# Optimization experiments

Measured on AMD Instinct MI355X. Metric: run time of the kernel, lower is better.

The kernel has to match this reference:

```python
import jax, jax.numpy as jnp
import numpy as np

N_NODES = 50000
N_EDGES = 800000
IN_DIM = 128
HID = 128
NUM_CLASSES = 2


def setup_inputs() -> dict:
    key = jax.random.key(0)
    ks = jax.random.split(key, 16)
    inp = {
        "adj_row": jax.random.randint(ks[0], (N_EDGES,), 0, N_NODES),
        "adj_col": jax.random.randint(ks[1], (N_EDGES,), 0, N_NODES),
        "adj_vals": jax.random.uniform(ks[2], (N_EDGES,), dtype=jnp.float32),
        "input_feature": jax.random.normal(ks[3], (N_NODES, IN_DIM), dtype=jnp.float32),
        "graph_indicator": jax.random.randint(ks[4], (N_NODES,), 0, 64),
        # GCN layer params (kaiming-uniform-ish init; zeros bias like the torch module)
        "W1": jax.random.uniform(ks[5], (IN_DIM, HID), jnp.float32, -1, 1) * np.sqrt(6.0 / IN_DIM),
        "b1": jnp.zeros((HID,), jnp.float32),
        "W2": jax.random.uniform(ks[6], (HID, HID), jnp.float32, -1, 1) * np.sqrt(6.0 / HID),
        "b2": jnp.zeros((HID,), jnp.float32),
        "W3": jax.random.uniform(ks[7], (HID, HID), jnp.float32, -1, 1) * np.sqrt(6.0 / HID),
        "b3": jnp.zeros((HID,), jnp.float32),
        # fc params (torch.nn.Linear default init range)
        "fcW1": jax.random.uniform(ks[8], (3 * HID, HID), jnp.float32, -1, 1) / np.sqrt(3 * HID),
        "fcb1": jax.random.uniform(ks[9], (HID,), jnp.float32, -1, 1) / np.sqrt(3 * HID),
        "fcW2": jax.random.uniform(ks[10], (HID, HID // 2), jnp.float32, -1, 1) / np.sqrt(HID),
        "fcb2": jax.random.uniform(ks[11], (HID // 2,), jnp.float32, -1, 1) / np.sqrt(HID),
        "fcW3": jax.random.uniform(ks[12], (HID // 2, NUM_CLASSES), jnp.float32, -1, 1) / np.sqrt(HID // 2),
        "fcb3": jax.random.uniform(ks[13], (NUM_CLASSES,), jnp.float32, -1, 1) / np.sqrt(HID // 2),
    }
    return inp


def _gcn_layer(row, col, vals, x, W, b, n_nodes):
    # support = X @ W  -> dense GEMM
    support = x @ W
    # sparse.mm(A, support): out[i] = sum_{e: row[e]=i} vals[e] * support[col[e]]
    msgs = support[col] * vals[:, None]  # [E, D] gather + scale
    agg = jax.ops.segment_sum(msgs, row, num_segments=n_nodes)
    return agg + b


def reference(adj_row, adj_col, adj_vals, input_feature, graph_indicator,
              W1, b1, W2, b2, W3, b3, fcW1, fcb1, fcW2, fcb2, fcW3, fcb3):
    n = input_feature.shape[0]
    g1 = jax.nn.relu(_gcn_layer(adj_row, adj_col, adj_vals, input_feature, W1, b1, n))
    g2 = jax.nn.relu(_gcn_layer(adj_row, adj_col, adj_vals, g1, W2, b2, n))
    g3 = jax.nn.relu(_gcn_layer(adj_row, adj_col, adj_vals, g2, W3, b3, n))
    feat = jnp.concatenate([g1, g2, g3], axis=1)  # [N, 3*HID]
    h = jax.nn.relu(feat @ fcW1 + fcb1)
    h = jax.nn.relu(h @ fcW2 + fcb2)
    logits = h @ fcW3 + fcb3
    return logits
```

## Files before the change

kernel.cpp:

```cpp
#include <hip/hip_runtime.h>
#include <hip/hip_bf16.h>

#define N_NODES 50000
#define N_EDGES 800000
#define NBK 391
#define BCAP 2560
#define PADSLACK 896

static inline int cdiv(int a, int b) { return (a + b - 1) / b; }

typedef __attribute__((ext_vector_type(8))) short short8;
typedef __attribute__((ext_vector_type(4))) float f32x4;

__device__ __forceinline__ float b2f(unsigned short u) {
    union { unsigned int i; float f; } c;
    c.i = ((unsigned int)u) << 16;
    return c.f;
}
__device__ __forceinline__ unsigned short f2bb(float f) {
    __hip_bfloat16 h = __float2bfloat16(f);
    return *(unsigned short*)&h;
}

__device__ __forceinline__ void pack_one(const float* __restrict__ W,
                                         __hip_bfloat16* __restrict__ out,
                                         int K, int N, int t) {
    int lane = t & 63;
    int kc = (t >> 6) % (K / 32);
    int nt = (t >> 6) / (K / 32);
    int kbase = kc * 32 + (lane >> 4) * 8;
    int col = nt * 16 + (lane & 15);
    __hip_bfloat16* dst = out + (size_t)t * 8;
#pragma unroll
    for (int j = 0; j < 8; ++j)
        dst[j] = __float2bfloat16(W[(size_t)(kbase + j) * N + col]);
}

__global__ __launch_bounds__(256)
void stage1_kernel(const int* __restrict__ row, const int* __restrict__ col,
                   const float* __restrict__ vals, int* __restrict__ bcursor,
                   int2* __restrict__ tmp, int E,
                   const float* __restrict__ x, __hip_bfloat16* __restrict__ support,
                   int M,
                   const float* __restrict__ W1, const float* __restrict__ W2,
                   const float* __restrict__ W3, const float* __restrict__ fcW1,
                   const float* __restrict__ fcW2,
                   __hip_bfloat16* __restrict__ pW2, __hip_bfloat16* __restrict__ pW3,
                   __hip_bfloat16* __restrict__ pfcW1, __hip_bfloat16* __restrict__ pfcW2) {
    __shared__ unsigned short As[64][136];
    __shared__ int hist[NBK];
    __shared__ int base[NBK];
    const int b = blockIdx.x;
    const int tid = threadIdx.x;

    if (b < 196) {
        const int CH = 4096;
        int e0 = b * CH;
        for (int i = tid; i < NBK; i += 256) hist[i] = 0;
        __syncthreads();
        for (int i = tid; i < CH; i += 256) {
            int e = e0 + i;
            if (e < E) atomicAdd(&hist[row[e] >> 7], 1);
        }
        __syncthreads();
        for (int i = tid; i < NBK; i += 256) {
            int c = hist[i];
            base[i] = (c > 0) ? (i * BCAP + atomicAdd(&bcursor[i], c)) : 0;
            hist[i] = 0;
        }
        __syncthreads();
        for (int i = tid; i < CH; i += 256) {
            int e = e0 + i;
            if (e < E) {
                int r = row[e];
                int bk = r >> 7;
                int rk = atomicAdd(&hist[bk], 1);
                tmp[base[bk] + rk] = make_int2(((r & 127) << 16) | col[e],
                                               __float_as_int(vals[e]));
            }
        }
        return;
    }

    if (b < 978) {
        const int wave = tid >> 6;
        const int lane = tid & 63;
        const int ln15 = lane & 15;
        const int quad = lane >> 4;
        const int m0 = (b - 196) * 64;

        short8 bfr[4][2];
#pragma unroll
        for (int kc = 0; kc < 4; ++kc)
#pragma unroll
            for (int h = 0; h < 2; ++h)
#pragma unroll
                for (int j = 0; j < 8; ++j)
                    bfr[kc][h][j] = (short)f2bb(
                        W1[(size_t)(kc * 32 + quad * 8 + j) * 128 + (wave * 2 + h) * 16 + ln15]);

#pragma unroll
        for (int i = 0; i < 4; ++i) {
            int idx = tid + i * 256;
            int r = idx >> 4;
            int c8 = (idx & 15) * 8;
            uint4 pk = {0, 0, 0, 0};
            if (m0 + r < M) {
                const float* src = &x[(size_t)(m0 + r) * 128 + c8];
                float4 a = *(const float4*)src;
                float4 bq = *(const float4*)(src + 4);
                pk.x = f2bb(a.x) | ((unsigned int)f2bb(a.y) << 16);
                pk.y = f2bb(a.z) | ((unsigned int)f2bb(a.w) << 16);
                pk.z = f2bb(bq.x) | ((unsigned int)f2bb(bq.y) << 16);
                pk.w = f2bb(bq.z) | ((unsigned int)f2bb(bq.w) << 16);
            }
            *(uint4*)&As[r][c8] = pk;
        }
        __syncthreads();

        f32x4 acc[4][2];
#pragma unroll
        for (int s = 0; s < 4; ++s)
#pragma unroll
            for (int h = 0; h < 2; ++h) acc[s][h] = (f32x4){0.f, 0.f, 0.f, 0.f};
#pragma unroll
        for (int kc = 0; kc < 4; ++kc) {
            short8 af[4];
#pragma unroll
            for (int s = 0; s < 4; ++s)
                af[s] = *(const short8*)&As[s * 16 + ln15][kc * 32 + quad * 8];
#pragma unroll
            for (int s = 0; s < 4; ++s)
#pragma unroll
                for (int h = 0; h < 2; ++h)
                    acc[s][h] = __builtin_amdgcn_mfma_f32_16x16x32_bf16(
                        af[s], bfr[kc][h], acc[s][h], 0, 0, 0);
        }
#pragma unroll
        for (int s = 0; s < 4; ++s)
#pragma unroll
            for (int h = 0; h < 2; ++h) {
                int cl = (wave * 2 + h) * 16 + ln15;
#pragma unroll
                for (int r = 0; r < 4; ++r) {
                    int rw = m0 + s * 16 + quad * 4 + r;
                    if (rw < M)
                        support[(size_t)rw * 128 + cl] = __float2bfloat16(acc[s][h][r]);
                }
            }
        return;
    }

    int pb = b - 978;
    if (pb < 8)       pack_one(W2,  pW2,  128, 128, pb * 256 + tid);
    else if (pb < 16) pack_one(W3,  pW3,  128, 128, (pb - 8) * 256 + tid);
    else if (pb < 40) pack_one(fcW1, pfcW1, 384, 128, (pb - 16) * 256 + tid);
    else              pack_one(fcW2, pfcW2, 128, 64, (pb - 40) * 256 + tid);
}

__global__ __launch_bounds__(256)
void binB_kernel(const int2* __restrict__ tmp, const int* __restrict__ bcursor,
                 int2* __restrict__ rowrange, int2* __restrict__ epack, int N) {
    int b = blockIdx.x;
    int r0 = b << 7;
    int nr = N - r0; if (nr > 128) nr = 128;
    __shared__ int cnt[128];
    __shared__ int cur[128];
    __shared__ int rpos[128];
    __shared__ int red[256];
    int t = threadIdx.x;
    int partial = 0;
    for (int i = t; i < b; i += 256) partial += bcursor[i];
    red[t] = partial;
    if (t < 128) cnt[t] = 0;
    __syncthreads();
    for (int off = 128; off > 0; off >>= 1) {
        if (t < off) red[t] += red[t + off];
        __syncthreads();
    }
    int slab = b * BCAP;
    int send = slab + bcursor[b];
    for (int i = slab + t; i < send; i += 256)
        atomicAdd(&cnt[tmp[i].x >> 16], 1);
    __syncthreads();
    int rcnt = (t < 128) ? cnt[t] : 0;
    int pc = (rcnt + 7) & ~7;
    if (t < 128) cur[t] = pc;
    __syncthreads();
    for (int off = 1; off < 128; off <<= 1) {
        int u = (t >= off && t < 128) ? cur[t - off] : 0;
        __syncthreads();
        if (t < 128) cur[t] += u;
        __syncthreads();
    }
    int obase = red[0] + b * PADSLACK;
    if (t < 128) {
        int pos = obase + cur[t] - pc;
        rpos[t] = pos;
        cur[t] = pos;
        if (t < nr) rowrange[r0 + t] = make_int2(pos, pos + pc);
    }
    __syncthreads();
    for (int i = slab + t; i < send; i += 256) {
        int2 v = tmp[i];
        int rl = v.x >> 16;
        int c = v.x & 0xffff;
        int pos = atomicAdd(&cur[rl], 1);
        epack[pos] = make_int2(c, v.y);
    }
    if (t < 128) {
        int rc = rcnt;
        int pos = rpos[t];
#pragma unroll 1
        for (int i = pos + rc; i < pos + pc; ++i)
            epack[i] = make_int2(0, 0);
    }
}

__device__ __forceinline__ void accum8(float* acc, long long e, uint4 u) {
    float f = __int_as_float((int)(e >> 32));
    acc[0] += f * b2f((unsigned short)(u.x & 0xffff));
    acc[1] += f * b2f((unsigned short)(u.x >> 16));
    acc[2] += f * b2f((unsigned short)(u.y & 0xffff));
    acc[3] += f * b2f((unsigned short)(u.y >> 16));
    acc[4] += f * b2f((unsigned short)(u.z & 0xffff));
    acc[5] += f * b2f((unsigned short)(u.z >> 16));
    acc[6] += f * b2f((unsigned short)(u.w & 0xffff));
    acc[7] += f * b2f((unsigned short)(u.w >> 16));
}

__device__ __forceinline__ void agg_node(const long long* __restrict__ ep,
                                         const __hip_bfloat16* __restrict__ support,
                                         int p, int end, int g, int j, float* acc) {
#pragma unroll
    for (int k = 0; k < 8; ++k) acc[k] = 0.f;
    long long e0 = 0, e1 = 0;
    uint4 u0 = {0, 0, 0, 0}, u1 = {0, 0, 0, 0};
    bool have = false;
    if (p < end) {
        e0 = ep[p + g];
        e1 = ep[p + 4 + g];
        u0 = *(const uint4*)&support[(size_t)(unsigned int)(e0 & 0xffffffffu) * 128 + j * 8];
        u1 = *(const uint4*)&support[(size_t)(unsigned int)(e1 & 0xffffffffu) * 128 + j * 8];
        p += 8;
        have = true;
    }
    while (p < end) {
        long long f0 = ep[p + g];
        long long f1 = ep[p + 4 + g];
        uint4 w0 = *(const uint4*)&support[(size_t)(unsigned int)(f0 & 0xffffffffu) * 128 + j * 8];
        uint4 w1 = *(const uint4*)&support[(size_t)(unsigned int)(f1 & 0xffffffffu) * 128 + j * 8];
        accum8(acc, e0, u0);
        accum8(acc, e1, u1);
        e0 = f0; u0 = w0; e1 = f1; u1 = w1;
        p += 8;
    }
    if (have) {
        accum8(acc, e0, u0);
        accum8(acc, e1, u1);
    }
#pragma unroll
    for (int k = 0; k < 8; ++k) {
        acc[k] += __shfl_xor(acc[k], 16);
        acc[k] += __shfl_xor(acc[k], 32);
    }
}

__global__ __launch_bounds__(512, 4)
void spmm_gemm_kernel(const int2* __restrict__ rowrange,
                      const int2* __restrict__ epack,
                      const __hip_bfloat16* __restrict__ support,
                      const float* __restrict__ bias,
                      __hip_bfloat16* __restrict__ gout,
                      const __hip_bfloat16* __restrict__ pW,
                      __hip_bfloat16* __restrict__ Cout,
                      int N) {
    __shared__ unsigned short As[64][136];
    const int tid = threadIdx.x;
    const int wv = tid >> 6;
    const int l = tid & 63;
    const int g = l >> 4;
    const int j = l & 15;
    const int m0 = blockIdx.x * 64;
    const long long* ep = (const long long*)epack;
    float4 b0 = *(const float4*)&bias[j * 8];
    float4 b1 = *(const float4*)&bias[j * 8 + 4];

    for (int i = 0; i < 8; ++i) {
        int node = m0 + wv * 8 + i;
        if (node >= N) {
            if (g == 0) *(uint4*)&As[wv * 8 + i][j * 8] = (uint4){0, 0, 0, 0};
            continue;
        }
        int2 rr = rowrange[node];
        float acc[8];
        agg_node(ep, support, rr.x, rr.y, g, j, acc);
        if (g == 0) {
            unsigned int q0 = (unsigned int)f2bb(fmaxf(acc[0] + b0.x, 0.f))
                            | ((unsigned int)f2bb(fmaxf(acc[1] + b0.y, 0.f)) << 16);
            unsigned int q1 = (unsigned int)f2bb(fmaxf(acc[2] + b0.z, 0.f))
                            | ((unsigned int)f2bb(fmaxf(acc[3] + b0.w, 0.f)) << 16);
            unsigned int q2 = (unsigned int)f2bb(fmaxf(acc[4] + b1.x, 0.f))
                            | ((unsigned int)f2bb(fmaxf(acc[5] + b1.y, 0.f)) << 16);
            unsigned int q3 = (unsigned int)f2bb(fmaxf(acc[6] + b1.z, 0.f))
                            | ((unsigned int)f2bb(fmaxf(acc[7] + b1.w, 0.f)) << 16);
            uint4 st = {q0, q1, q2, q3};
            *(uint4*)&As[wv * 8 + i][j * 8] = st;
            *(uint4*)&gout[(size_t)(m0 + wv * 8 + i) * 384 + j * 8] = st;
        }
    }
    __syncthreads();

    const int ln15 = l & 15;
    const int quad = l >> 4;
    f32x4 acc2[4];
#pragma unroll
    for (int s = 0; s < 4; ++s) acc2[s] = (f32x4){0.f, 0.f, 0.f, 0.f};
#pragma unroll
    for (int kc = 0; kc < 4; ++kc) {
        short8 af[4];
#pragma unroll
        for (int s = 0; s < 4; ++s)
            af[s] = *(const short8*)&As[s * 16 + ln15][kc * 32 + quad * 8];
        short8 bf = *(const short8*)&pW[((size_t)(wv * 4 + kc) * 64 + l) * 8];
#pragma unroll
        for (int s = 0; s < 4; ++s)
            acc2[s] = __builtin_amdgcn_mfma_f32_16x16x32_bf16(af[s], bf, acc2[s], 0, 0, 0);
    }
    {
        int cl = wv * 16 + ln15;
#pragma unroll
        for (int s = 0; s < 4; ++s)
#pragma unroll
            for (int r = 0; r < 4; ++r) {
                int rw = m0 + s * 16 + quad * 4 + r;
                if (rw < N)
                    Cout[(size_t)rw * 128 + cl] = __float2bfloat16(acc2[s][r]);
            }
    }
}

__global__ __launch_bounds__(512, 4)
void spmm_fc_kernel(const int2* __restrict__ rowrange,
                    const int2* __restrict__ epack,
                    const __hip_bfloat16* __restrict__ support,
                    const float* __restrict__ bias,
                    const __hip_bfloat16* __restrict__ featb,
                    const __hip_bfloat16* __restrict__ pfcW1,
                    const float* __restrict__ fcb1,
                    const __hip_bfloat16* __restrict__ pfcW2,
                    const float* __restrict__ fcb2,
                    const float* __restrict__ fcW3, const float* __restrict__ fcb3,
                    float* __restrict__ out, int N) {
    __shared__ unsigned short As[64][136];
    __shared__ float w3s[128];
    __shared__ float b3s[2];
    const int tid = threadIdx.x;
    const int wv = tid >> 6;
    const int l = tid & 63;
    const int g = l >> 4;
    const int j = l & 15;
    const int m0 = blockIdx.x * 64;
    const long long* ep = (const long long*)epack;
    if (tid < 128) w3s[tid] = fcW3[tid];
    if (tid < 2) b3s[tid] = fcb3[tid];
    float4 b0 = *(const float4*)&bias[j * 8];
    float4 b1 = *(const float4*)&bias[j * 8 + 4];

    for (int i = 0; i < 8; ++i) {
        int node = m0 + wv * 8 + i;
        if (node >= N) {
            if (g == 0) *(uint4*)&As[wv * 8 + i][j * 8] = (uint4){0, 0, 0, 0};
            continue;
        }
        int2 rr = rowrange[node];
        float acc[8];
        agg_node(ep, support, rr.x, rr.y, g, j, acc);
        if (g == 0) {
            unsigned int q0 = (unsigned int)f2bb(fmaxf(acc[0] + b0.x, 0.f))
                            | ((unsigned int)f2bb(fmaxf(acc[1] + b0.y, 0.f)) << 16);
            unsigned int q1 = (unsigned int)f2bb(fmaxf(acc[2] + b0.z, 0.f))
                            | ((unsigned int)f2bb(fmaxf(acc[3] + b0.w, 0.f)) << 16);
            unsigned int q2 = (unsigned int)f2bb(fmaxf(acc[4] + b1.x, 0.f))
                            | ((unsigned int)f2bb(fmaxf(acc[5] + b1.y, 0.f)) << 16);
            unsigned int q3 = (unsigned int)f2bb(fmaxf(acc[6] + b1.z, 0.f))
                            | ((unsigned int)f2bb(fmaxf(acc[7] + b1.w, 0.f)) << 16);
            uint4 st = {q0, q1, q2, q3};
            *(uint4*)&As[wv * 8 + i][j * 8] = st;
        }
    }
    __syncthreads();

    const int ln15 = l & 15;
    const int quad = l >> 4;
    f32x4 acc[4];
#pragma unroll
    for (int s = 0; s < 4; ++s) acc[s] = (f32x4){0.f, 0.f, 0.f, 0.f};
#pragma unroll
    for (int step = 0; step < 3; ++step) {
        const int kb = (step == 0) ? 2 : (step - 1);
        if (step != 0) {
            __syncthreads();
#pragma unroll
            for (int i = 0; i < 2; ++i) {
                int idx = tid + i * 512;
                int r = idx >> 4;
                int c8 = (idx & 15) * 8;
                uint4 v = *(const uint4*)&featb[(size_t)(m0 + r) * 384 + kb * 128 + c8];
                *(uint4*)&As[r][c8] = v;
            }
            __syncthreads();
        }
#pragma unroll
        for (int kc = 0; kc < 4; ++kc) {
            short8 af[4];
#pragma unroll
            for (int s = 0; s < 4; ++s)
                af[s] = *(const short8*)&As[s * 16 + ln15][kc * 32 + quad * 8];
            int kcg = kb * 4 + kc;
            short8 bf = *(const short8*)&pfcW1[((size_t)(wv * 12 + kcg) * 64 + l) * 8];
#pragma unroll
            for (int s = 0; s < 4; ++s)
                acc[s] = __builtin_amdgcn_mfma_f32_16x16x32_bf16(af[s], bf, acc[s], 0, 0, 0);
        }
    }
    __syncthreads();
    {
        int col = wv * 16 + ln15;
        float bv = fcb1[col];
#pragma unroll
        for (int s = 0; s < 4; ++s)
#pragma unroll
            for (int r = 0; r < 4; ++r) {
                int row = s * 16 + quad * 4 + r;
                As[row][col] = f2bb(fmaxf(acc[s][r] + bv, 0.f));
            }
    }
    __syncthreads();

    if (wv < 4) {
        f32x4 acc2[4];
#pragma unroll
        for (int s = 0; s < 4; ++s) acc2[s] = (f32x4){0.f, 0.f, 0.f, 0.f};
#pragma unroll
        for (int kc = 0; kc < 4; ++kc) {
            short8 af[4];
#pragma unroll
            for (int s = 0; s < 4; ++s)
                af[s] = *(const short8*)&As[s * 16 + ln15][kc * 32 + quad * 8];
            short8 bfw = *(const short8*)&pfcW2[((size_t)(wv * 4 + kc) * 64 + l) * 8];
#pragma unroll
            for (int s = 0; s < 4; ++s)
                acc2[s] = __builtin_amdgcn_mfma_f32_16x16x32_bf16(af[s], bfw, acc2[s], 0, 0, 0);
        }
        __syncthreads();
        int col2 = wv * 16 + ln15;
        float bv = fcb2[col2];
#pragma unroll
        for (int s = 0; s < 4; ++s)
#pragma unroll
            for (int r = 0; r < 4; ++r) {
                int row = s * 16 + quad * 4 + r;
                As[row][col2] = f2bb(fmaxf(acc2[s][r] + bv, 0.f));
            }
    } else {
        __syncthreads();
    }
    __syncthreads();

    if (tid < 128) {
        int row = tid >> 1, cls = tid & 1;
        int grow = m0 + row;
        if (grow < N) {
            float a = b3s[cls];
#pragma unroll
            for (int k = 0; k < 64; ++k)
                a += b2f(As[row][k]) * w3s[k * 2 + cls];
            out[(size_t)grow * 2 + cls] = a;
        }
    }
}

extern "C" void kernel_launch(void* const* d_in, const int* in_sizes, int n_in,
                              void* d_out, int out_size, void* d_ws, size_t ws_size,
                              hipStream_t stream) {
    const int*   adj_row  = (const int*)d_in[0];
    const int*   adj_col  = (const int*)d_in[1];
    const float* adj_vals = (const float*)d_in[2];
    const float* x        = (const float*)d_in[3];
    const float* W1   = (const float*)d_in[5];
    const float* b1   = (const float*)d_in[6];
    const float* W2   = (const float*)d_in[7];
    const float* b2   = (const float*)d_in[8];
    const float* W3   = (const float*)d_in[9];
    const float* b3   = (const float*)d_in[10];
    const float* fcW1 = (const float*)d_in[11];
    const float* fcb1 = (const float*)d_in[12];
    const float* fcW2 = (const float*)d_in[13];
    const float* fcb2 = (const float*)d_in[14];
    const float* fcW3 = (const float*)d_in[15];
    const float* fcb3 = (const float*)d_in[16];
    float* out = (float*)d_out;

    const int N = N_NODES, E = N_EDGES;
    const int Mpad = 50048;
    const int EPAD = E + NBK * PADSLACK + 64;

    char* p = (char*)d_ws;
    auto alloc = [&](size_t bytes) {
        char* q = p;
        p += (bytes + 255) & ~(size_t)255;
        return q;
    };
    __hip_bfloat16* featb    = (__hip_bfloat16*)alloc((size_t)Mpad * 384 * 2);
    __hip_bfloat16* supportb = (__hip_bfloat16*)alloc((size_t)Mpad * 128 * 2);
    __hip_bfloat16* supportc = (__hip_bfloat16*)alloc((size_t)Mpad * 128 * 2);
    __hip_bfloat16* pW2   = (__hip_bfloat16*)alloc(16384 * 2);
    __hip_bfloat16* pW3   = (__hip_bfloat16*)alloc(16384 * 2);
    __hip_bfloat16* pfcW1 = (__hip_bfloat16*)alloc(49152 * 2);
    __hip_bfloat16* pfcW2 = (__hip_bfloat16*)alloc(8192 * 2);
    int2*  rowrange  = (int2*)alloc((size_t)(N + 1) * 8);
    int*   bcursor   = (int*)alloc((size_t)NBK * 4);
    int2*  epack     = (int2*)alloc((size_t)EPAD * 8);
    int2*  tmp       = (int2*)alloc((size_t)NBK * BCAP * 8);

    hipMemsetAsync(bcursor, 0, (size_t)NBK * 4, stream);
    stage1_kernel<<<1022, 256, 0, stream>>>(adj_row, adj_col, adj_vals, bcursor, tmp, E,
                                            x, supportb, N,
                                            W1, W2, W3, fcW1, fcW2,
                                            pW2, pW3, pfcW1, pfcW2);
    binB_kernel<<<NBK, 256, 0, stream>>>(tmp, bcursor, rowrange, epack, N);

    const int fgrid = cdiv(N, 64);

    spmm_gemm_kernel<<<fgrid, 512, 0, stream>>>(rowrange, epack, supportb, b1,
                                                featb + 0, pW2, supportc, N);
    spmm_gemm_kernel<<<fgrid, 512, 0, stream>>>(rowrange, epack, supportc, b2,
                                                featb + 128, pW3, supportb, N);
    spmm_fc_kernel<<<fgrid, 512, 0, stream>>>(rowrange, epack, supportb, b3,
                                              featb, pfcW1, fcb1, pfcW2, fcb2,
                                              fcW3, fcb3, out, N);
}
```

Before: 280.4 us.

## Shrink fused SpMM+GEMM row tile from 64 to 16 nodes per block

The fused aggregation plus dense-GEMM kernels now process 16 nodes per 256-thread block instead of 64 nodes per 512-thread block. The MFMA work is redistributed so each wave computes two 16-column tiles over a single 16-row tile. Smaller blocks mean less time lost at the block-wide barrier waiting for slow, high-degree nodes, a smaller tail, and more blocks resident per CU. The cost is that each block reloads weight fragments for fewer rows, adding global weight traffic per node.

```diff
diff --git a/kernel.cpp b/kernel.cpp
--- a/kernel.cpp
+++ b/kernel.cpp
@@ -266,7 +266,7 @@
     }
 }
 
-__global__ __launch_bounds__(512, 4)
+__global__ __launch_bounds__(256, 8)
 void spmm_gemm_kernel(const int2* __restrict__ rowrange,
                       const int2* __restrict__ epack,
                       const __hip_bfloat16* __restrict__ support,
@@ -275,72 +275,70 @@
                       const __hip_bfloat16* __restrict__ pW,
                       __hip_bfloat16* __restrict__ Cout,
                       int N) {
-    __shared__ unsigned short As[64][136];
+    __shared__ unsigned short As[16][136];
     const int tid = threadIdx.x;
     const int wv = tid >> 6;
     const int l = tid & 63;
     const int g = l >> 4;
     const int j = l & 15;
-    const int m0 = blockIdx.x * 64;
+    const int m0 = blockIdx.x * 16;
     const long long* ep = (const long long*)epack;
     float4 b0 = *(const float4*)&bias[j * 8];
     float4 b1 = *(const float4*)&bias[j * 8 + 4];
 
-    for (int i = 0; i < 8; ++i) {
-        int node = m0 + wv * 8 + i;
-        if (node >= N) {
-            if (g == 0) *(uint4*)&As[wv * 8 + i][j * 8] = (uint4){0, 0, 0, 0};
-            continue;
-        }
-        int2 rr = rowrange[node];
-        float acc[8];
-        agg_node(ep, support, rr.x, rr.y, g, j, acc);
-        if (g == 0) {
-            unsigned int q0 = (unsigned int)f2bb(fmaxf(acc[0] + b0.x, 0.f))
-                            | ((unsigned int)f2bb(fmaxf(acc[1] + b0.y, 0.f)) << 16);
-            unsigned int q1 = (unsigned int)f2bb(fmaxf(acc[2] + b0.z, 0.f))
-                            | ((unsigned int)f2bb(fmaxf(acc[3] + b0.w, 0.f)) << 16);
-            unsigned int q2 = (unsigned int)f2bb(fmaxf(acc[4] + b1.x, 0.f))
-                            | ((unsigned int)f2bb(fmaxf(acc[5] + b1.y, 0.f)) << 16);
-            unsigned int q3 = (unsigned int)f2bb(fmaxf(acc[6] + b1.z, 0.f))
-                            | ((unsigned int)f2bb(fmaxf(acc[7] + b1.w, 0.f)) << 16);
-            uint4 st = {q0, q1, q2, q3};
-            *(uint4*)&As[wv * 8 + i][j * 8] = st;
-            *(uint4*)&gout[(size_t)(m0 + wv * 8 + i) * 384 + j * 8] = st;
+    for (int i = 0; i < 4; ++i) {
+        int node = m0 + wv * 4 + i;
+        if (node < N) {
+            int2 rr = rowrange[node];
+            float acc[8];
+            agg_node(ep, support, rr.x, rr.y, g, j, acc);
+            if (g == 0) {
+                unsigned int q0 = (unsigned int)f2bb(fmaxf(acc[0] + b0.x, 0.f))
+                                | ((unsigned int)f2bb(fmaxf(acc[1] + b0.y, 0.f)) << 16);
+                unsigned int q1 = (unsigned int)f2bb(fmaxf(acc[2] + b0.z, 0.f))
+                                | ((unsigned int)f2bb(fmaxf(acc[3] + b0.w, 0.f)) << 16);
+                unsigned int q2 = (unsigned int)f2bb(fmaxf(acc[4] + b1.x, 0.f))
+                                | ((unsigned int)f2bb(fmaxf(acc[5] + b1.y, 0.f)) << 16);
+                unsigned int q3 = (unsigned int)f2bb(fmaxf(acc[6] + b1.z, 0.f))
+                                | ((unsigned int)f2bb(fmaxf(acc[7] + b1.w, 0.f)) << 16);
+                uint4 st = {q0, q1, q2, q3};
+                *(uint4*)&As[wv * 4 + i][j * 8] = st;
+                *(uint4*)&gout[(size_t)node * 384 + j * 8] = st;
+            }
+        } else if (g == 0) {
+            *(uint4*)&As[wv * 4 + i][j * 8] = (uint4){0, 0, 0, 0};
         }
     }
     __syncthreads();
 
     const int ln15 = l & 15;
     const int quad = l >> 4;
-    f32x4 acc2[4];
-#pragma unroll
-    for (int s = 0; s < 4; ++s) acc2[s] = (f32x4){0.f, 0.f, 0.f, 0.f};
+    f32x4 acc2[2];
+    acc2[0] = (f32x4){0.f, 0.f, 0.f, 0.f};
+    acc2[1] = (f32x4){0.f, 0.f, 0.f, 0.f};
 #pragma unroll
     for (int kc = 0; kc < 4; ++kc) {
-        short8 af[4];
-#pragma unroll
-        for (int s = 0; s < 4; ++s)
-            af[s] = *(const short8*)&As[s * 16 + ln15][kc * 32 + quad * 8];
-        short8 bf = *(const short8*)&pW[((size_t)(wv * 4 + kc) * 64 + l) * 8];
-#pragma unroll
-        for (int s = 0; s < 4; ++s)
-            acc2[s] = __builtin_amdgcn_mfma_f32_16x16x32_bf16(af[s], bf, acc2[s], 0, 0, 0);
-    }
-    {
-        int cl = wv * 16 + ln15;
-#pragma unroll
-        for (int s = 0; s < 4; ++s)
-#pragma unroll
-            for (int r = 0; r < 4; ++r) {
-                int rw = m0 + s * 16 + quad * 4 + r;
-                if (rw < N)
-                    Cout[(size_t)rw * 128 + cl] = __float2bfloat16(acc2[s][r]);
-            }
-    }
-}
-
-__global__ __launch_bounds__(512, 4)
+        short8 af = *(const short8*)&As[ln15][kc * 32 + quad * 8];
+#pragma unroll
+        for (int h = 0; h < 2; ++h) {
+            int nt = wv * 2 + h;
+            short8 bf = *(const short8*)&pW[((size_t)(nt * 4 + kc) * 64 + l) * 8];
+            acc2[h] = __builtin_amdgcn_mfma_f32_16x16x32_bf16(af, bf, acc2[h], 0, 0, 0);
+        }
+    }
+#pragma unroll
+    for (int h = 0; h < 2; ++h) {
+        int cl = (wv * 2 + h) * 16 + ln15;
+#pragma unroll
+        for (int r = 0; r < 4; ++r) {
+            int rw = m0 + quad * 4 + r;
+            if (rw < N)
+                Cout[(size_t)rw * 128 + cl] = __float2bfloat16(acc2[h][r]);
+        }
+    }
+}
+
+__global__ __launch_bounds__(256, 8)
 void spmm_fc_kernel(const int2* __restrict__ rowrange,
                     const int2* __restrict__ epack,
                     const __hip_bfloat16* __restrict__ support,
@@ -352,7 +350,7 @@
                     const float* __restrict__ fcb2,
                     const float* __restrict__ fcW3, const float* __restrict__ fcb3,
                     float* __restrict__ out, int N) {
-    __shared__ unsigned short As[64][136];
+    __shared__ unsigned short As[16][136];
     __shared__ float w3s[128];
     __shared__ float b3s[2];
     const int tid = threadIdx.x;
@@ -360,115 +358,94 @@
     const int l = tid & 63;
     const int g = l >> 4;
     const int j = l & 15;
-    const int m0 = blockIdx.x * 64;
+    const int m0 = blockIdx.x * 16;
     const long long* ep = (const long long*)epack;
     if (tid < 128) w3s[tid] = fcW3[tid];
     if (tid < 2) b3s[tid] = fcb3[tid];
     float4 b0 = *(const float4*)&bias[j * 8];
     float4 b1 = *(const float4*)&bias[j * 8 + 4];
 
-    for (int i = 0; i < 8; ++i) {
-        int node = m0 + wv * 8 + i;
-        if (node >= N) {
-            if (g == 0) *(uint4*)&As[wv * 8 + i][j * 8] = (uint4){0, 0, 0, 0};
-            continue;
-        }
-        int2 rr = rowrange[node];
-        float acc[8];
-        agg_node(ep, support, rr.x, rr.y, g, j, acc);
-        if (g == 0) {
-            unsigned int q0 = (unsigned int)f2bb(fmaxf(acc[0] + b0.x, 0.f))
-                            | ((unsigned int)f2bb(fmaxf(acc[1] + b0.y, 0.f)) << 16);
-            unsigned int q1 = (unsigned int)f2bb(fmaxf(acc[2] + b0.z, 0.f))
-                            | ((unsigned int)f2bb(fmaxf(acc[3] + b0.w, 0.f)) << 16);
-            unsigned int q2 = (unsigned int)f2bb(fmaxf(acc[4] + b1.x, 0.f))
-                            | ((unsigned int)f2bb(fmaxf(acc[5] + b1.y, 0.f)) << 16);
-            unsigned int q3 = (unsigned int)f2bb(fmaxf(acc[6] + b1.z, 0.f))
-                            | ((unsigned int)f2bb(fmaxf(acc[7] + b1.w, 0.f)) << 16);
-            uint4 st = {q0, q1, q2, q3};
-            *(uint4*)&As[wv * 8 + i][j * 8] = st;
+    for (int i = 0; i < 4; ++i) {
+        int node = m0 + wv * 4 + i;
+        if (node < N) {
+            int2 rr = rowrange[node];
+            float acc[8];
+            agg_node(ep, support, rr.x, rr.y, g, j, acc);
+            if (g == 0) {
+                unsigned int q0 = (unsigned int)f2bb(fmaxf(acc[0] + b0.x, 0.f))
+                                | ((unsigned int)f2bb(fmaxf(acc[1] + b0.y, 0.f)) << 16);
+                unsigned int q1 = (unsigned int)f2bb(fmaxf(acc[2] + b0.z, 0.f))
+                                | ((unsigned int)f2bb(fmaxf(acc[3] + b0.w, 0.f)) << 16);
+                unsigned int q2 = (unsigned int)f2bb(fmaxf(acc[4] + b1.x, 0.f))
+                                | ((unsigned int)f2bb(fmaxf(acc[5] + b1.y, 0.f)) << 16);
+                unsigned int q3 = (unsigned int)f2bb(fmaxf(acc[6] + b1.z, 0.f))
+                                | ((unsigned int)f2bb(fmaxf(acc[7] + b1.w, 0.f)) << 16);
+                uint4 st = {q0, q1, q2, q3};
+                *(uint4*)&As[wv * 4 + i][j * 8] = st;
+            }
+        } else if (g == 0) {
+            *(uint4*)&As[wv * 4 + i][j * 8] = (uint4){0, 0, 0, 0};
         }
     }
     __syncthreads();
 
     const int ln15 = l & 15;
     const int quad = l >> 4;
-    f32x4 acc[4];
-#pragma unroll
-    for (int s = 0; s < 4; ++s) acc[s] = (f32x4){0.f, 0.f, 0.f, 0.f};
+    f32x4 acc[2];
+    acc[0] = (f32x4){0.f, 0.f, 0.f, 0.f};
+    acc[1] = (f32x4){0.f, 0.f, 0.f, 0.f};
 #pragma unroll
     for (int step = 0; step < 3; ++step) {
         const int kb = (step == 0) ? 2 : (step - 1);
         if (step != 0) {
             __syncthreads();
-#pragma unroll
-            for (int i = 0; i < 2; ++i) {
-                int idx = tid + i * 512;
-                int r = idx >> 4;
-                int c8 = (idx & 15) * 8;
-                uint4 v = *(const uint4*)&featb[(size_t)(m0 + r) * 384 + kb * 128 + c8];
-                *(uint4*)&As[r][c8] = v;
+            int r = tid >> 4;
+            int c8 = (tid & 15) * 8;
+            *(uint4*)&As[r][c8] =
+                *(const uint4*)&featb[(size_t)(m0 + r) * 384 + kb * 128 + c8];
+            __syncthreads();
+        }
+#pragma unroll
+        for (int kc = 0; kc < 4; ++kc) {
+            short8 af = *(const short8*)&As[ln15][kc * 32 + quad * 8];
+            int kcg = kb * 4 + kc;
+#pragma unroll
+            for (int h = 0; h < 2; ++h) {
+                int nt = wv * 2 + h;
+                short8 bf = *(const short8*)&pfcW1[((size_t)(nt * 12 + kcg) * 64 + l) * 8];
+                acc[h] = __builtin_amdgcn_mfma_f32_16x16x32_bf16(af, bf, acc[h], 0, 0, 0);
             }
-            __syncthreads();
-        }
-#pragma unroll
-        for (int kc = 0; kc < 4; ++kc) {
-            short8 af[4];
-#pragma unroll
-            for (int s = 0; s < 4; ++s)
-                af[s] = *(const short8*)&As[s * 16 + ln15][kc * 32 + quad * 8];
-            int kcg = kb * 4 + kc;
-            short8 bf = *(const short8*)&pfcW1[((size_t)(wv * 12 + kcg) * 64 + l) * 8];
-#pragma unroll
-            for (int s = 0; s < 4; ++s)
-                acc[s] = __builtin_amdgcn_mfma_f32_16x16x32_bf16(af[s], bf, acc[s], 0, 0, 0);
-        }
+        }
+    }
+    __syncthreads();
+#pragma unroll
+    for (int h = 0; h < 2; ++h) {
+        int col = (wv * 2 + h) * 16 + ln15;
+        float bv = fcb1[col];
+#pragma unroll
+        for (int r = 0; r < 4; ++r)
+            As[quad * 4 + r][col] = f2bb(fmaxf(acc[h][r] + bv, 0.f));
+    }
+    __syncthreads();
+
+    f32x4 acc2 = (f32x4){0.f, 0.f, 0.f, 0.f};
+#pragma unroll
+    for (int kc = 0; kc < 4; ++kc) {
+        short8 af = *(const short8*)&As[ln15][kc * 32 + quad * 8];
+        short8 bfw = *(const short8*)&pfcW2[((size_t)(wv * 4 + kc) * 64 + l) * 8];
+        acc2 = __builtin_amdgcn_mfma_f32_16x16x32_bf16(af, bfw, acc2, 0, 0, 0);
     }
     __syncthreads();
     {
-        int col = wv * 16 + ln15;
-        float bv = fcb1[col];
-#pragma unroll
-        for (int s = 0; s < 4; ++s)
-#pragma unroll
-            for (int r = 0; r < 4; ++r) {
-                int row = s * 16 + quad * 4 + r;
-                As[row][col] = f2bb(fmaxf(acc[s][r] + bv, 0.f));
-            }
-    }
-    __syncthreads();
-
-    if (wv < 4) {
-        f32x4 acc2[4];
-#pragma unroll
-        for (int s = 0; s < 4; ++s) acc2[s] = (f32x4){0.f, 0.f, 0.f, 0.f};
-#pragma unroll
-        for (int kc = 0; kc < 4; ++kc) {
-            short8 af[4];
-#pragma unroll
-            for (int s = 0; s < 4; ++s)
-                af[s] = *(const short8*)&As[s * 16 + ln15][kc * 32 + quad * 8];
-            short8 bfw = *(const short8*)&pfcW2[((size_t)(wv * 4 + kc) * 64 + l) * 8];
-#pragma unroll
-            for (int s = 0; s < 4; ++s)
-                acc2[s] = __builtin_amdgcn_mfma_f32_16x16x32_bf16(af[s], bfw, acc2[s], 0, 0, 0);
-        }
-        __syncthreads();
         int col2 = wv * 16 + ln15;
         float bv = fcb2[col2];
 #pragma unroll
-        for (int s = 0; s < 4; ++s)
-#pragma unroll
-            for (int r = 0; r < 4; ++r) {
-                int row = s * 16 + quad * 4 + r;
-                As[row][col2] = f2bb(fmaxf(acc2[s][r] + bv, 0.f));
-            }
-    } else {
-        __syncthreads();
-    }
-    __syncthreads();
-
-    if (tid < 128) {
+        for (int r = 0; r < 4; ++r)
+            As[quad * 4 + r][col2] = f2bb(fmaxf(acc2[r] + bv, 0.f));
+    }
+    __syncthreads();
+
+    if (tid < 32) {
         int row = tid >> 1, cls = tid & 1;
         int grow = m0 + row;
         if (grow < N) {
@@ -531,13 +508,13 @@
                                             pW2, pW3, pfcW1, pfcW2);
     binB_kernel<<<NBK, 256, 0, stream>>>(tmp, bcursor, rowrange, epack, N);
 
-    const int fgrid = cdiv(N, 64);
-
-    spmm_gemm_kernel<<<fgrid, 512, 0, stream>>>(rowrange, epack, supportb, b1,
+    const int fgrid = cdiv(N, 16);
+
+    spmm_gemm_kernel<<<fgrid, 256, 0, stream>>>(rowrange, epack, supportb, b1,
                                                 featb + 0, pW2, supportc, N);
-    spmm_gemm_kernel<<<fgrid, 512, 0, stream>>>(rowrange, epack, supportc, b2,
+    spmm_gemm_kernel<<<fgrid, 256, 0, stream>>>(rowrange, epack, supportc, b2,
                                                 featb + 128, pW3, supportb, N);
-    spmm_fc_kernel<<<fgrid, 512, 0, stream>>>(rowrange, epack, supportb, b3,
+    spmm_fc_kernel<<<fgrid, 256, 0, stream>>>(rowrange, epack, supportb, b3,
                                               featb, pfcW1, fcb1, pfcW2, fcb2,
                                               fcW3, fcb3, out, N);
 }
```

Result: faster. 250.4 us (-10.7%).
